# Kernel optimization log

Measured on AMD Instinct MI355X. Metric: run time of the kernel, lower is better.

## Reference

```python
import jax, jax.numpy as jnp
import numpy as np

B, S, E, H = 4, 2048, 2048, 16
D = E // H  # head_dim = 128
MAX_LEN = 2048


def _make_freqs():
    # standard RoPE frequencies: theta = 10000^{-2i/D}
    inv_freq = 1.0 / (10000.0 ** (np.arange(0, D, 2, dtype=np.float32) / D))  # [D/2]
    t = np.arange(MAX_LEN, dtype=np.float32)
    ang = np.outer(t, inv_freq)  # [max_len, D/2]
    cos = ang.reshape(1, MAX_LEN, 1, D // 2)
    return jnp.asarray(np.cos(cos)), jnp.asarray(np.sin(cos))


def setup_inputs() -> dict:
    key = jax.random.key(0)
    ks = jax.random.split(key, 10)
    sc = 1.0 / np.sqrt(E)
    freqs_cos, freqs_sin = _make_freqs()
    return {
        "x": jax.random.normal(ks[0], (B, S, E), dtype=jnp.float32),
        "freqs_cos": freqs_cos,
        "freqs_sin": freqs_sin,
        "wq": jax.random.normal(ks[1], (E, E), dtype=jnp.float32) * sc,
        "bq": jax.random.normal(ks[2], (E,), dtype=jnp.float32) * 0.01,
        "wk": jax.random.normal(ks[3], (E, E), dtype=jnp.float32) * sc,
        "bk": jax.random.normal(ks[4], (E,), dtype=jnp.float32) * 0.01,
        "wv": jax.random.normal(ks[5], (E, E), dtype=jnp.float32) * sc,
        "bv": jax.random.normal(ks[6], (E,), dtype=jnp.float32) * 0.01,
        "wo": jax.random.normal(ks[7], (E, E), dtype=jnp.float32) * sc,
        "bo": jax.random.normal(ks[8], (E,), dtype=jnp.float32) * 0.01,
    }


def _rope(t, cos, sin):
    # t: [B, S, H, D]; complex multiply on interleaved (even, odd) pairs
    tr = t.reshape(*t.shape[:-1], -1, 2)  # [B,S,H,D/2,2]
    xr, xi = tr[..., 0], tr[..., 1]
    rr = xr * cos - xi * sin
    ri = xr * sin + xi * cos
    return jnp.stack([rr, ri], axis=-1).reshape(t.shape)


def reference(x, freqs_cos, freqs_sin, wq, bq, wk, bk, wv, bv, wo, bo):
    b, s, _ = x.shape
    q = (x @ wq.T + bq).reshape(b, s, H, D)
    k = (x @ wk.T + bk).reshape(b, s, H, D)
    v = (x @ wv.T + bv).reshape(b, s, H, D)
    cos, sin = freqs_cos[:, :s], freqs_sin[:, :s]
    q = _rope(q, cos, sin)
    k = _rope(k, cos, sin)
    # FAITHFUL to source: q,k,v stay [B,S,H,D], so matmul contracts over D
    # producing per-position head-head scores [B,S,H,H] (no transpose to BHSD).
    qk = jnp.einsum("bshd,bsgd->bshg", q, k) / jnp.sqrt(jnp.float32(D))
    att = jax.nn.softmax(qk, axis=-1)
    att_out = jnp.einsum("bshg,bsgd->bshd", att, v)  # [B,S,H,D]
    # torch: transpose(1,2).contiguous().view(B,S,-1) -> h-major flatten
    att_out = jnp.transpose(att_out, (0, 2, 1, 3)).reshape(b, s, -1)
    return att_out @ wo.T + bo
```

## Files before the change

kernel.cpp:

```cpp
#include <hip/hip_runtime.h>
#include <stdint.h>

typedef unsigned short u16t;
typedef __attribute__((ext_vector_type(8))) short frag8;
typedef __attribute__((ext_vector_type(4))) float facc4;

#define S_LEN 2048
#define E_DIM 2048

__device__ __forceinline__ u16t f2bf(float f) {
    union { float f; uint32_t u; } c; c.f = f;
    return (u16t)((c.u + 0x7fffu + ((c.u >> 16) & 1u)) >> 16);
}

__global__ __launch_bounds__(256) void cvt_kernel(const float* __restrict__ src,
                                                  u16t* __restrict__ dst, int n4) {
    int i = blockIdx.x * 256 + threadIdx.x;
    if (i >= n4) return;
    float4 v = ((const float4*)src)[i];
    ushort4 o;
    o.x = f2bf(v.x); o.y = f2bf(v.y); o.z = f2bf(v.z); o.w = f2bf(v.w);
    ((ushort4*)dst)[i] = o;
}

__device__ __forceinline__ void gldl16(const u16t* g, u16t* l) {
    __builtin_amdgcn_global_load_lds(
        (__attribute__((address_space(1))) void*)(g),
        (__attribute__((address_space(3))) void*)(l), 16, 0, 0);
}

__device__ __forceinline__ void gemm_core(const u16t* __restrict__ A,
                                          const u16t* __restrict__ Bw,
                                          u16t* As0, u16t* As1,
                                          u16t* Bs0, u16t* Bs1,
                                          facc4 acc[4][4]) {
    const int t    = threadIdx.x;
    const int lane = t & 63;
    const int wid  = t >> 6;
    const int m16  = lane & 15;
    const int quad = lane >> 4;
    const int wm   = (wid & 1) * 64;
    const int wn   = (wid >> 1) * 64;
    const size_t bm0 = (size_t)blockIdx.y * 128;
    const size_t bn0 = (size_t)blockIdx.x * 128;

#pragma unroll
    for (int i = 0; i < 4; ++i)
#pragma unroll
        for (int j = 0; j < 4; ++j) acc[i][j] = facc4{0.f, 0.f, 0.f, 0.f};

    const u16t* Ab = A + bm0 * E_DIM;
    const u16t* Bb = Bw + bn0 * E_DIM;

    const int e0 = wid * 512;
    const int e1 = 2048 + wid * 512;
    const int le0 = e0 + lane * 8, le1 = e1 + lane * 8;
    const int r0 = le0 >> 5, c0 = le0 & 31;
    const int r1 = le1 >> 5, c1 = le1 & 31;
    const size_t ga0 = (size_t)r0 * E_DIM + c0;
    const size_t ga1 = (size_t)r1 * E_DIM + c1;

    for (int k0 = 0; k0 < E_DIM; k0 += 64) {
        __syncthreads();
        gldl16(Ab + ga0 + k0,      As0 + e0);
        gldl16(Ab + ga1 + k0,      As0 + e1);
        gldl16(Ab + ga0 + k0 + 32, As1 + e0);
        gldl16(Ab + ga1 + k0 + 32, As1 + e1);
        gldl16(Bb + ga0 + k0,      Bs0 + e0);
        gldl16(Bb + ga1 + k0,      Bs0 + e1);
        gldl16(Bb + ga0 + k0 + 32, Bs1 + e0);
        gldl16(Bb + ga1 + k0 + 32, Bs1 + e1);
        __syncthreads();

#pragma unroll
        for (int h = 0; h < 2; ++h) {
            const u16t* Ah = h ? As1 : As0;
            const u16t* Bh = h ? Bs1 : Bs0;
            frag8 av[4], bv[4];
#pragma unroll
            for (int i = 0; i < 4; ++i)
                av[i] = *(const frag8*)(Ah + (wm + i * 16 + m16) * 32 + quad * 8);
#pragma unroll
            for (int j = 0; j < 4; ++j)
                bv[j] = *(const frag8*)(Bh + (wn + j * 16 + m16) * 32 + quad * 8);
#pragma unroll
            for (int i = 0; i < 4; ++i)
#pragma unroll
                for (int j = 0; j < 4; ++j)
                    acc[i][j] = __builtin_amdgcn_mfma_f32_16x16x32_bf16(
                        av[i], bv[j], acc[i][j], 0, 0, 0);
        }
    }
}

struct QkvArgs {
    const u16t* w[3];
    const float* bias[3];
    u16t* out[3];
};

__global__ __launch_bounds__(256, 2)
void qkv_gemm(const u16t* __restrict__ xb, QkvArgs args,
              const float* __restrict__ fcos, const float* __restrict__ fsin) {
    __shared__ u16t As0[128 * 32], As1[128 * 32];
    __shared__ u16t Bs0[128 * 32], Bs1[128 * 32];
    facc4 acc[4][4];
    const int z = blockIdx.z;
    gemm_core(xb, args.w[z], As0, As1, Bs0, Bs1, acc);

    const int t    = threadIdx.x;
    const int lane = t & 63;
    const int m16  = lane & 15;
    const int quad = lane >> 4;
    const int wid  = t >> 6;
    const int wm   = (wid & 1) * 64;
    const int wn   = (wid >> 1) * 64;
    const int bm0  = blockIdx.y * 128;
    const int bn0  = blockIdx.x * 128;
    const bool rope = (z < 2);
    u16t* out = args.out[z];
    const float* bias = args.bias[z];

#pragma unroll
    for (int i = 0; i < 4; ++i) {
#pragma unroll
        for (int j = 0; j < 4; ++j) {
            const int n = bn0 + wn + j * 16 + m16;
            const float bn_ = bias[n];
#pragma unroll
            for (int r = 0; r < 4; ++r) {
                const int m = bm0 + wm + i * 16 + quad * 4 + r;
                float v = acc[i][j][r] + bn_;
                const float part = __shfl_xor(v, 1, 64);
                if (rope) {
                    const int s = m & (S_LEN - 1);
                    const int p = (n & 127) >> 1;
                    const float cs = fcos[s * 64 + p];
                    const float sn = fsin[s * 64 + p];
                    v = (n & 1) ? (part * sn + v * cs) : (v * cs - part * sn);
                }
                out[(size_t)m * E_DIM + n] = f2bf(v);
            }
        }
    }
}

__global__ __launch_bounds__(256, 2)
void out_gemm(const u16t* __restrict__ sh, const u16t* __restrict__ wob,
              const float* __restrict__ bo, float* __restrict__ out) {
    __shared__ u16t As0[128 * 32], As1[128 * 32];
    __shared__ u16t Bs0[128 * 32], Bs1[128 * 32];
    facc4 acc[4][4];
    gemm_core(sh, wob, As0, As1, Bs0, Bs1, acc);

    const int t    = threadIdx.x;
    const int lane = t & 63;
    const int m16  = lane & 15;
    const int quad = lane >> 4;
    const int wid  = t >> 6;
    const int wm   = (wid & 1) * 64;
    const int wn   = (wid >> 1) * 64;
    const int bm0  = blockIdx.y * 128;
    const int bn0  = blockIdx.x * 128;

#pragma unroll
    for (int i = 0; i < 4; ++i) {
#pragma unroll
        for (int j = 0; j < 4; ++j) {
            const int n = bn0 + wn + j * 16 + m16;
            const float bn_ = bo[n];
#pragma unroll
            for (int r = 0; r < 4; ++r) {
                const int m = bm0 + wm + i * 16 + quad * 4 + r;
                out[(size_t)m * E_DIM + n] = acc[i][j][r] + bn_;
            }
        }
    }
}

__global__ __launch_bounds__(256)
void attn_kernel(const u16t* __restrict__ qb, const u16t* __restrict__ kb,
                 const u16t* __restrict__ vb, u16t* __restrict__ sh) {
    __shared__ u16t Vs[4][16 * 136];
    __shared__ u16t Pt[4][16 * 32];

    const int t    = threadIdx.x;
    const int wid  = t >> 6;
    const int lane = t & 63;
    const int m16  = lane & 15;
    const int quad = lane >> 4;
    const int tk   = blockIdx.x * 4 + wid;
    const int b    = tk >> 11;
    const int s    = tk & (S_LEN - 1);
    const size_t row = (size_t)tk * E_DIM;

    frag8 aq[4], ak[4];
    const u16t* qrow = qb + row + m16 * 128 + quad * 8;
    const u16t* krow = kb + row + m16 * 128 + quad * 8;
#pragma unroll
    for (int ks = 0; ks < 4; ++ks) {
        aq[ks] = *(const frag8*)(qrow + ks * 32);
        ak[ks] = *(const frag8*)(krow + ks * 32);
    }

    u16t* vs = Vs[wid];
#pragma unroll
    for (int c = 0; c < 4; ++c) {
        const int e  = c * 512 + lane * 8;
        const int vr = e >> 7, vc = e & 127;
        *(uint4*)(vs + vr * 136 + vc) = *(const uint4*)(vb + row + e);
    }

    facc4 sacc = facc4{0.f, 0.f, 0.f, 0.f};
#pragma unroll
    for (int ks = 0; ks < 4; ++ks)
        sacc = __builtin_amdgcn_mfma_f32_16x16x32_bf16(aq[ks], ak[ks], sacc, 0, 0, 0);

    float p[4], mx[4], sm[4];
#pragma unroll
    for (int r = 0; r < 4; ++r) { p[r] = sacc[r] * 0.08838834764831845f; mx[r] = p[r]; }
#pragma unroll
    for (int msk = 1; msk < 16; msk <<= 1)
#pragma unroll
        for (int r = 0; r < 4; ++r) mx[r] = fmaxf(mx[r], __shfl_xor(mx[r], msk, 64));
#pragma unroll
    for (int r = 0; r < 4; ++r) { p[r] = __expf(p[r] - mx[r]); sm[r] = p[r]; }
#pragma unroll
    for (int msk = 1; msk < 16; msk <<= 1)
#pragma unroll
        for (int r = 0; r < 4; ++r) sm[r] += __shfl_xor(sm[r], msk, 64);

    u16t* pt = Pt[wid];
#pragma unroll
    for (int r = 0; r < 4; ++r)
        pt[(quad * 4 + r) * 32 + m16] = f2bf(p[r] / sm[r]);
    *(uint2*)(pt + m16 * 32 + 16 + quad * 4) = uint2{0u, 0u};

    __syncthreads();

    const frag8 aP = *(const frag8*)(pt + m16 * 32 + quad * 8);

    facc4 oacc[8];
#pragma unroll
    for (int d = 0; d < 8; ++d) oacc[d] = facc4{0.f, 0.f, 0.f, 0.f};
#pragma unroll
    for (int dblk = 0; dblk < 8; ++dblk) {
        union { u16t u[8]; frag8 f; } bb;
#pragma unroll
        for (int j = 0; j < 8; ++j)
            bb.u[j] = vs[((quad * 8 + j) & 15) * 136 + dblk * 16 + m16];
        oacc[dblk] = __builtin_amdgcn_mfma_f32_16x16x32_bf16(aP, bb.f, oacc[dblk], 0, 0, 0);
    }

    const size_t base = ((size_t)b << 22) + (size_t)(s >> 4) * E_DIM
                      + (size_t)((s & 15) * 128);
#pragma unroll
    for (int dblk = 0; dblk < 8; ++dblk) {
        const int d = dblk * 16 + m16;
#pragma unroll
        for (int r = 0; r < 4; ++r) {
            const int h = quad * 4 + r;
            sh[base + ((size_t)h << 18) + d] = f2bf(oacc[dblk][r]);
        }
    }
}

extern "C" void kernel_launch(void* const* d_in, const int* in_sizes, int n_in,
                              void* d_out, int out_size, void* d_ws, size_t ws_size,
                              hipStream_t stream) {
    const float* x    = (const float*)d_in[0];
    const float* fcos = (const float*)d_in[1];
    const float* fsin = (const float*)d_in[2];
    const float* wq   = (const float*)d_in[3];
    const float* bq   = (const float*)d_in[4];
    const float* wk   = (const float*)d_in[5];
    const float* bk   = (const float*)d_in[6];
    const float* wv   = (const float*)d_in[7];
    const float* bv   = (const float*)d_in[8];
    const float* wo   = (const float*)d_in[9];
    const float* bo   = (const float*)d_in[10];
    float* out = (float*)d_out;

    char* ws = (char*)d_ws;
    u16t* xb  = (u16t*)(ws);
    u16t* qb  = (u16t*)(ws + 33554432ull);
    u16t* kb  = (u16t*)(ws + 67108864ull);
    u16t* vb  = (u16t*)(ws + 100663296ull);
    u16t* wqb = (u16t*)(ws + 134217728ull);
    u16t* wkb = (u16t*)(ws + 142606336ull);
    u16t* wvb = (u16t*)(ws + 150994944ull);
    u16t* wob = (u16t*)(ws + 159383552ull);

    cvt_kernel<<<16384, 256, 0, stream>>>(x, xb, 4194304);
    cvt_kernel<<<4096, 256, 0, stream>>>(wq, wqb, 1048576);
    cvt_kernel<<<4096, 256, 0, stream>>>(wk, wkb, 1048576);
    cvt_kernel<<<4096, 256, 0, stream>>>(wv, wvb, 1048576);
    cvt_kernel<<<4096, 256, 0, stream>>>(wo, wob, 1048576);

    QkvArgs qa;
    qa.w[0] = wqb; qa.w[1] = wkb; qa.w[2] = wvb;
    qa.bias[0] = bq; qa.bias[1] = bk; qa.bias[2] = bv;
    qa.out[0] = qb; qa.out[1] = kb; qa.out[2] = vb;
    qkv_gemm<<<dim3(16, 64, 3), 256, 0, stream>>>(xb, qa, fcos, fsin);

    attn_kernel<<<2048, 256, 0, stream>>>(qb, kb, vb, xb);

    out_gemm<<<dim3(16, 64), 256, 0, stream>>>(xb, wob, bo, out);
}
```

Before: 520.0 us.

## Widen GEMM tiles to 128x256 and XOR-swizzle LDS layout

Doubles the N dimension of the block tile in both the QKV and output GEMMs, so each wave computes a 64x128 sub-tile with 32 accumulators, and halves the grid along N. This raises arithmetic intensity per LDS and global load. It also adds an XOR swizzle on the 16-byte column chunks in LDS to reduce bank conflicts on fragment reads. In exchange the kernel needs more registers and shared memory, which may lower occupancy under the launch bound of 2 blocks, and there are fewer blocks to spread across CUs.

```diff
diff --git a/kernel.cpp b/kernel.cpp
--- a/kernel.cpp
+++ b/kernel.cpp
@@ -33,60 +33,74 @@
                                           const u16t* __restrict__ Bw,
                                           u16t* As0, u16t* As1,
                                           u16t* Bs0, u16t* Bs1,
-                                          facc4 acc[4][4]) {
+                                          facc4 acc[4][8]) {
     const int t    = threadIdx.x;
     const int lane = t & 63;
     const int wid  = t >> 6;
     const int m16  = lane & 15;
     const int quad = lane >> 4;
+    const int sw   = (m16 >> 1) & 3;
     const int wm   = (wid & 1) * 64;
-    const int wn   = (wid >> 1) * 64;
+    const int wn   = (wid >> 1) * 128;
     const size_t bm0 = (size_t)blockIdx.y * 128;
-    const size_t bn0 = (size_t)blockIdx.x * 128;
+    const size_t bn0 = (size_t)blockIdx.x * 256;
 
 #pragma unroll
     for (int i = 0; i < 4; ++i)
 #pragma unroll
-        for (int j = 0; j < 4; ++j) acc[i][j] = facc4{0.f, 0.f, 0.f, 0.f};
+        for (int j = 0; j < 8; ++j) acc[i][j] = facc4{0.f, 0.f, 0.f, 0.f};
 
     const u16t* Ab = A + bm0 * E_DIM;
     const u16t* Bb = Bw + bn0 * E_DIM;
 
-    const int e0 = wid * 512;
-    const int e1 = 2048 + wid * 512;
-    const int le0 = e0 + lane * 8, le1 = e1 + lane * 8;
-    const int r0 = le0 >> 5, c0 = le0 & 31;
-    const int r1 = le1 >> 5, c1 = le1 & 31;
-    const size_t ga0 = (size_t)r0 * E_DIM + c0;
-    const size_t ga1 = (size_t)r1 * E_DIM + c1;
+    const int l8 = lane * 8;
+    const int rA0 = ((wid * 1024 + l8) >> 5);
+    const int rA1 = rA0 + 16;
+    const int rB0 = ((wid * 2048 + l8) >> 5);
+    const int rB1 = rB0 + 16, rB2 = rB0 + 32, rB3 = rB0 + 48;
+    const int c3 = lane & 3;
+    const size_t gA0 = (size_t)rA0 * E_DIM + ((c3 ^ ((rA0 >> 1) & 3)) * 8);
+    const size_t gA1 = (size_t)rA1 * E_DIM + ((c3 ^ ((rA1 >> 1) & 3)) * 8);
+    const size_t gB0 = (size_t)rB0 * E_DIM + ((c3 ^ ((rB0 >> 1) & 3)) * 8);
+    const size_t gB1 = (size_t)rB1 * E_DIM + ((c3 ^ ((rB1 >> 1) & 3)) * 8);
+    const size_t gB2 = (size_t)rB2 * E_DIM + ((c3 ^ ((rB2 >> 1) & 3)) * 8);
+    const size_t gB3 = (size_t)rB3 * E_DIM + ((c3 ^ ((rB3 >> 1) & 3)) * 8);
+    u16t* lA0 = As0 + wid * 1024;
+    u16t* lA1 = As1 + wid * 1024;
+    u16t* lB0 = Bs0 + wid * 2048;
+    u16t* lB1 = Bs1 + wid * 2048;
 
     for (int k0 = 0; k0 < E_DIM; k0 += 64) {
         __syncthreads();
-        gldl16(Ab + ga0 + k0,      As0 + e0);
-        gldl16(Ab + ga1 + k0,      As0 + e1);
-        gldl16(Ab + ga0 + k0 + 32, As1 + e0);
-        gldl16(Ab + ga1 + k0 + 32, As1 + e1);
-        gldl16(Bb + ga0 + k0,      Bs0 + e0);
-        gldl16(Bb + ga1 + k0,      Bs0 + e1);
-        gldl16(Bb + ga0 + k0 + 32, Bs1 + e0);
-        gldl16(Bb + ga1 + k0 + 32, Bs1 + e1);
+        gldl16(Ab + gA0 + k0,      lA0);
+        gldl16(Ab + gA1 + k0,      lA0 + 512);
+        gldl16(Ab + gA0 + k0 + 32, lA1);
+        gldl16(Ab + gA1 + k0 + 32, lA1 + 512);
+        gldl16(Bb + gB0 + k0,      lB0);
+        gldl16(Bb + gB1 + k0,      lB0 + 512);
+        gldl16(Bb + gB2 + k0,      lB0 + 1024);
+        gldl16(Bb + gB3 + k0,      lB0 + 1536);
+        gldl16(Bb + gB0 + k0 + 32, lB1);
+        gldl16(Bb + gB1 + k0 + 32, lB1 + 512);
+        gldl16(Bb + gB2 + k0 + 32, lB1 + 1024);
+        gldl16(Bb + gB3 + k0 + 32, lB1 + 1536);
         __syncthreads();
 
 #pragma unroll
         for (int h = 0; h < 2; ++h) {
             const u16t* Ah = h ? As1 : As0;
             const u16t* Bh = h ? Bs1 : Bs0;
-            frag8 av[4], bv[4];
+            frag8 av[4], bv[8];
 #pragma unroll
             for (int i = 0; i < 4; ++i)
-                av[i] = *(const frag8*)(Ah + (wm + i * 16 + m16) * 32 + quad * 8);
-#pragma unroll
-            for (int j = 0; j < 4; ++j)
-                bv[j] = *(const frag8*)(Bh + (wn + j * 16 + m16) * 32 + quad * 8);
+                av[i] = *(const frag8*)(Ah + (wm + i * 16 + m16) * 32 + (quad ^ sw) * 8);
+#pragma unroll
+            for (int j = 0; j < 8; ++j)
+                bv[j] = *(const frag8*)(Bh + (wn + j * 16 + m16) * 32 + (quad ^ sw) * 8);
 #pragma unroll
             for (int i = 0; i < 4; ++i)
 #pragma unroll
-                for (int j = 0; j < 4; ++j)
+                for (int j = 0; j < 8; ++j)
                     acc[i][j] = __builtin_amdgcn_mfma_f32_16x16x32_bf16(
                         av[i], bv[j], acc[i][j], 0, 0, 0);
         }
@@ -103,8 +117,8 @@
 void qkv_gemm(const u16t* __restrict__ xb, QkvArgs args,
               const float* __restrict__ fcos, const float* __restrict__ fsin) {
     __shared__ u16t As0[128 * 32], As1[128 * 32];
-    __shared__ u16t Bs0[128 * 32], Bs1[128 * 32];
-    facc4 acc[4][4];
+    __shared__ u16t Bs0[256 * 32], Bs1[256 * 32];
+    facc4 acc[4][8];
     const int z = blockIdx.z;
     gemm_core(xb, args.w[z], As0, As1, Bs0, Bs1, acc);
 
@@ -114,9 +128,9 @@
     const int quad = lane >> 4;
     const int wid  = t >> 6;
     const int wm   = (wid & 1) * 64;
-    const int wn   = (wid >> 1) * 64;
+    const int wn   = (wid >> 1) * 128;
     const int bm0  = blockIdx.y * 128;
-    const int bn0  = blockIdx.x * 128;
+    const int bn0  = blockIdx.x * 256;
     const bool rope = (z < 2);
     u16t* out = args.out[z];
     const float* bias = args.bias[z];
@@ -124,7 +138,7 @@
 #pragma unroll
     for (int i = 0; i < 4; ++i) {
 #pragma unroll
-        for (int j = 0; j < 4; ++j) {
+        for (int j = 0; j < 8; ++j) {
             const int n = bn0 + wn + j * 16 + m16;
             const float bn_ = bias[n];
 #pragma unroll
@@ -149,8 +163,8 @@
 void out_gemm(const u16t* __restrict__ sh, const u16t* __restrict__ wob,
               const float* __restrict__ bo, float* __restrict__ out) {
     __shared__ u16t As0[128 * 32], As1[128 * 32];
-    __shared__ u16t Bs0[128 * 32], Bs1[128 * 32];
-    facc4 acc[4][4];
+    __shared__ u16t Bs0[256 * 32], Bs1[256 * 32];
+    facc4 acc[4][8];
     gemm_core(sh, wob, As0, As1, Bs0, Bs1, acc);
 
     const int t    = threadIdx.x;
@@ -159,14 +173,14 @@
     const int quad = lane >> 4;
     const int wid  = t >> 6;
     const int wm   = (wid & 1) * 64;
-    const int wn   = (wid >> 1) * 64;
+    const int wn   = (wid >> 1) * 128;
     const int bm0  = blockIdx.y * 128;
-    const int bn0  = blockIdx.x * 128;
+    const int bn0  = blockIdx.x * 256;
 
 #pragma unroll
     for (int i = 0; i < 4; ++i) {
 #pragma unroll
-        for (int j = 0; j < 4; ++j) {
+        for (int j = 0; j < 8; ++j) {
             const int n = bn0 + wn + j * 16 + m16;
             const float bn_ = bo[n];
 #pragma unroll
@@ -301,9 +315,9 @@
     qa.w[0] = wqb; qa.w[1] = wkb; qa.w[2] = wvb;
     qa.bias[0] = bq; qa.bias[1] = bk; qa.bias[2] = bv;
     qa.out[0] = qb; qa.out[1] = kb; qa.out[2] = vb;
-    qkv_gemm<<<dim3(16, 64, 3), 256, 0, stream>>>(xb, qa, fcos, fsin);
+    qkv_gemm<<<dim3(8, 64, 3), 256, 0, stream>>>(xb, qa, fcos, fsin);
 
     attn_kernel<<<2048, 256, 0, stream>>>(qb, kb, vb, xb);
 
-    out_gemm<<<dim3(16, 64), 256, 0, stream>>>(xb, wob, bo, out);
-}
+    out_gemm<<<dim3(8, 64), 256, 0, stream>>>(xb, wob, bo, out);
+}
```

After: 526.2 us. No clear change (+1.2%).
